# Optimization experiments

Hardware: AMD Instinct MI355X
Metric: run time of the kernel (lower is better)

The kernel has to match this reference:

```python
import jax, jax.numpy as jnp
import numpy as np

NUM_HEADS = 12


def setup_inputs() -> dict:
    key = jax.random.key(0)
    ks = jax.random.split(key, 6)
    C = 768
    hd = C // NUM_HEADS  # 64
    H = W = 32
    x = jax.random.normal(ks[0], (4, H, W, C), dtype=jnp.float32)
    # Linear weights stored as (in, out) so y = x @ W (+ b)
    Wqkv = jax.random.normal(ks[1], (C, 3 * C), dtype=jnp.float32) * 0.02
    Wproj = jax.random.normal(ks[2], (C, C), dtype=jnp.float32) * 0.02
    bproj = jax.random.normal(ks[3], (C,), dtype=jnp.float32) * 0.02
    rel_pos_h = jax.random.normal(ks[4], (2 * H - 1, hd), dtype=jnp.float32) * 0.02
    rel_pos_w = jax.random.normal(ks[5], (2 * W - 1, hd), dtype=jnp.float32) * 0.02
    return {"x": x, "Wqkv": Wqkv, "Wproj": Wproj, "bproj": bproj,
            "rel_pos_h": rel_pos_h, "rel_pos_w": rel_pos_w}


def _get_rel_pos(size: int, rel_pos: jnp.ndarray) -> jnp.ndarray:
    # q_size == k_size == size; table already has 2*size-1 entries -> no interpolation
    coords = jnp.arange(size)[:, None] - jnp.arange(size)[None, :] + (size - 1)
    return rel_pos[coords]  # (size, size, head_dim)


def reference(x, Wqkv, Wproj, bproj, rel_pos_h, rel_pos_w):
    B, H, W, C = x.shape
    hn = NUM_HEADS
    hd = C // hn
    scale = hd ** (-0.5)
    S = H * W

    qkv = x @ Wqkv                                   # (B,H,W,3C)
    qkv = qkv.reshape(B, S, 3, hn, hd)
    qkv = jnp.transpose(qkv, (2, 0, 3, 1, 4)).reshape(3, B * hn, S, hd)
    q, k, v = qkv[0], qkv[1], qkv[2]                 # each (B*hn, S, hd)

    # decomposed relative position bias
    Rh = _get_rel_pos(H, rel_pos_h)                  # (H,H,hd)
    Rw = _get_rel_pos(W, rel_pos_w)                  # (W,W,hd)
    r_q = q.reshape(B * hn, H, W, hd)
    rel_h = jnp.einsum('bhwc,hkc->bhwk', r_q, Rh)    # (B*hn,H,W,H)
    rel_w = jnp.einsum('bhwc,wkc->bhwk', r_q, Rw)    # (B*hn,H,W,W)
    bias = rel_h[..., :, None] + rel_w[..., None, :] # (B*hn,H,W,H,W)
    bias = bias.reshape(B * hn, S, S)

    scores = scale * jnp.einsum('bqc,bkc->bqk', q, k) + bias
    attn = jax.nn.softmax(scores, axis=-1)
    out = jnp.einsum('bqk,bkc->bqc', attn, v)        # (B*hn,S,hd)

    out = out.reshape(B, hn, H, W, hd)
    out = jnp.transpose(out, (0, 2, 3, 1, 4)).reshape(B, H, W, C)
    return out @ Wproj + bproj
```

## Files before the change

kernel.cpp:

```cpp
#include <hip/hip_runtime.h>
#include <stddef.h>

typedef __bf16 bf16x8 __attribute__((ext_vector_type(8)));
typedef __bf16 bf16x4 __attribute__((ext_vector_type(4)));
typedef _Float16 f16x4 __attribute__((ext_vector_type(4)));
typedef float  f32x4  __attribute__((ext_vector_type(4)));

#define MFMA16(a, b, c) __builtin_amdgcn_mfma_f32_16x16x32_bf16((a), (b), (c), 0, 0, 0)
#define MFMA16H(a, b, c) __builtin_amdgcn_mfma_f32_16x16x16f16((a), (b), (c), 0, 0, 0)

__device__ __forceinline__ void gload_lds16(const void* gsrc, void* ldst) {
    __builtin_amdgcn_global_load_lds(
        (__attribute__((address_space(1))) void*)gsrc,
        (__attribute__((address_space(3))) void*)ldst,
        16, 0, 0);
}

__global__ void prep_kernel(const float* __restrict__ x, __bf16* __restrict__ xbf,
                            const float* __restrict__ Wqkv, __bf16* __restrict__ WqkvT,
                            const float* __restrict__ Wproj, __bf16* __restrict__ WprojT) {
    __shared__ float tile[32][33];
    const int bx = blockIdx.x, tid = threadIdx.x;
    if (bx < 3072) {
        int i = bx * 256 + tid;
        float4 v = ((const float4*)x)[i];
        bf16x4 o = {(__bf16)v.x, (__bf16)v.y, (__bf16)v.z, (__bf16)v.w};
        ((bf16x4*)xbf)[i] = o;
        return;
    }
    const float* in; __bf16* out; int R, C, c0, r0;
    if (bx < 4800) { int bb = bx - 3072; in = Wqkv;  out = WqkvT;  R = 768; C = 2304;
                     c0 = (bb % 72) * 32; r0 = (bb / 72) * 32; }
    else           { int bb = bx - 4800; in = Wproj; out = WprojT; R = 768; C = 768;
                     c0 = (bb % 24) * 32; r0 = (bb / 24) * 32; }
    const int tx = tid & 31, ty = tid >> 5;
#pragma unroll
    for (int i = 0; i < 32; i += 8)
        tile[ty + i][tx] = in[(size_t)(r0 + ty + i) * C + c0 + tx];
    __syncthreads();
#pragma unroll
    for (int i = 0; i < 32; i += 8)
        out[(size_t)(c0 + ty + i) * R + r0 + tx] = (__bf16)tile[tx][ty + i];
}

__device__ __forceinline__ void gemm_core_bk64(
    const __bf16* __restrict__ A, const __bf16* __restrict__ Bt, int K,
    int m0, int n0, __bf16* aT, __bf16* bT, f32x4 acc[4][4]) {
    const int tid  = threadIdx.x;
    const int wid  = tid >> 6, lane = tid & 63;
    const int quad = lane >> 4, l16 = lane & 15;
    const int wm = (wid >> 1) * 64, wn = (wid & 1) * 64;
    const int r_in = lane >> 3;
    const int cswz = ((lane & 7) ^ r_in) * 8;
    const __bf16* gA = A  + (size_t)(m0 + wid * 8 + r_in) * K + cswz;
    const __bf16* gB = Bt + (size_t)(n0 + wid * 8 + r_in) * K + cswz;
    const int sA = (l16 & 7);
    for (int k0 = 0; k0 < K; k0 += 64) {
        __syncthreads();
#pragma unroll
        for (int j = 0; j < 4; j++) {
            gload_lds16(gA + (size_t)(j * 32) * K + k0, aT + (j * 32 + wid * 8) * 64);
            gload_lds16(gB + (size_t)(j * 32) * K + k0, bT + (j * 32 + wid * 8) * 64);
        }
        __syncthreads();
#pragma unroll
        for (int kh = 0; kh < 2; kh++) {
            bf16x8 af[4], bfr[4];
#pragma unroll
            for (int t = 0; t < 4; t++) {
                const int slot = ((kh * 4 + quad) ^ sA) << 3;
                af[t]  = *(const bf16x8*)(aT + (wm + t * 16 + l16) * 64 + slot);
                bfr[t] = *(const bf16x8*)(bT + (wn + t * 16 + l16) * 64 + slot);
            }
#pragma unroll
            for (int rt = 0; rt < 4; rt++)
#pragma unroll
                for (int ct = 0; ct < 4; ct++)
                    acc[rt][ct] = MFMA16(af[rt], bfr[ct], acc[rt][ct]);
        }
    }
}

__global__ __launch_bounds__(256, 3)
void gemm_qkv_kernel(const __bf16* __restrict__ A, const __bf16* __restrict__ Bt,
                     __bf16* __restrict__ qb, __bf16* __restrict__ kb,
                     _Float16* __restrict__ vtb) {
    __shared__ __bf16 aT[8192], bT[8192];
    f32x4 acc[4][4];
#pragma unroll
    for (int i = 0; i < 4; i++)
#pragma unroll
        for (int j = 0; j < 4; j++) { f32x4 z = {0.f, 0.f, 0.f, 0.f}; acc[i][j] = z; }
    const int m0 = blockIdx.x * 128, n0 = blockIdx.y * 128;
    gemm_core_bk64(A, Bt, 768, m0, n0, aT, bT, acc);
    const int tid = threadIdx.x, wid = tid >> 6, lane = tid & 63;
    const int quad = lane >> 4, l16 = lane & 15;
    const int wm = (wid >> 1) * 64, wn = (wid & 1) * 64;
#pragma unroll
    for (int rt = 0; rt < 4; rt++)
#pragma unroll
        for (int ct = 0; ct < 4; ct++) {
            const int ng = n0 + wn + ct * 16 + l16;
            const int which = ng / 768;
            const int rem = ng - which * 768;
            const int hh = rem >> 6, d = rem & 63;
#pragma unroll
            for (int r = 0; r < 4; r++) {
                const int mg = m0 + wm + rt * 16 + quad * 4 + r;
                const int b = mg >> 10, s = mg & 1023;
                const int bh = b * 12 + hh;
                if (which == 0)      qb[((size_t)bh * 1024 + s) * 64 + d] = (__bf16)acc[rt][ct][r];
                else if (which == 1) kb[((size_t)bh * 1024 + s) * 64 + d] = (__bf16)acc[rt][ct][r];
                else                 vtb[((size_t)bh * 64 + d) * 1024 + s] = (_Float16)acc[rt][ct][r];
            }
        }
}

__global__ __launch_bounds__(256, 3)
void gemm_proj_kernel(const __bf16* __restrict__ A, const __bf16* __restrict__ Bt,
                      const float* __restrict__ bias, float* __restrict__ out) {
    __shared__ __bf16 aT[8192], bT[8192];
    f32x4 acc[4][4];
#pragma unroll
    for (int i = 0; i < 4; i++)
#pragma unroll
        for (int j = 0; j < 4; j++) { f32x4 z = {0.f, 0.f, 0.f, 0.f}; acc[i][j] = z; }
    const int m0 = blockIdx.x * 128, n0 = blockIdx.y * 128;
    gemm_core_bk64(A, Bt, 768, m0, n0, aT, bT, acc);
    const int tid = threadIdx.x, wid = tid >> 6, lane = tid & 63;
    const int quad = lane >> 4, l16 = lane & 15;
    const int wm = (wid >> 1) * 64, wn = (wid & 1) * 64;
#pragma unroll
    for (int rt = 0; rt < 4; rt++)
#pragma unroll
        for (int ct = 0; ct < 4; ct++) {
            const int ng = n0 + wn + ct * 16 + l16;
            const float bb = bias[ng];
#pragma unroll
            for (int r = 0; r < 4; r++) {
                const int mg = m0 + wm + rt * 16 + quad * 4 + r;
                out[(size_t)mg * 768 + ng] = acc[rt][ct][r] + bb;
            }
        }
}

__global__ __launch_bounds__(256, 3)
void attn_kernel(const __bf16* __restrict__ q, const __bf16* __restrict__ kk,
                 const _Float16* __restrict__ vt, const float* __restrict__ rph,
                 const float* __restrict__ rpw, __bf16* __restrict__ aout) {
    __shared__ __bf16   kbuf2[2][4096];
    __shared__ _Float16 vbuf2[2][4096];
    __shared__ float    relh[64][33];
    const int tid = threadIdx.x, wid = tid >> 6, lane = tid & 63;
    const int quad = lane >> 4, l16 = lane & 15;
    const int bh = blockIdx.x, qt = blockIdx.y;
    const int b = bh / 12, hh = bh - b * 12;
    const int q0 = qt * 64;
    const int w0 = wid * 16;
    const int h = qt * 2 + (wid >> 1);

    const __bf16* qp = q + ((size_t)bh * 1024 + q0 + w0 + l16) * 64;
    bf16x8 aq0 = *(const bf16x8*)(qp + quad * 8);
    bf16x8 aq1 = *(const bf16x8*)(qp + 32 + quad * 8);

    float* Dw = ((float*)kbuf2) + wid * 1024;
#pragma unroll
    for (int ct = 0; ct < 4; ct++) {
        int j = ct * 16 + l16; if (j > 62) j = 62;
        const float* tb = rpw + (size_t)j * 64;
        float4 t0 = *(const float4*)(tb + quad * 8);
        float4 t1 = *(const float4*)(tb + quad * 8 + 4);
        float4 t2 = *(const float4*)(tb + 32 + quad * 8);
        float4 t3 = *(const float4*)(tb + 32 + quad * 8 + 4);
        bf16x8 b0 = {(__bf16)t0.x, (__bf16)t0.y, (__bf16)t0.z, (__bf16)t0.w,
                     (__bf16)t1.x, (__bf16)t1.y, (__bf16)t1.z, (__bf16)t1.w};
        bf16x8 b1 = {(__bf16)t2.x, (__bf16)t2.y, (__bf16)t2.z, (__bf16)t2.w,
                     (__bf16)t3.x, (__bf16)t3.y, (__bf16)t3.z, (__bf16)t3.w};
        f32x4 z = {0.f, 0.f, 0.f, 0.f};
        z = MFMA16(aq0, b0, z);
        z = MFMA16(aq1, b1, z);
#pragma unroll
        for (int i = 0; i < 4; i++)
            Dw[(quad * 4 + i) * 64 + ct * 16 + l16] = z[i];
    }
#pragma unroll
    for (int ct = 0; ct < 2; ct++) {
        const int tr = h - (ct * 16 + l16) + 31;
        const float* tb = rph + (size_t)tr * 64;
        float4 t0 = *(const float4*)(tb + quad * 8);
        float4 t1 = *(const float4*)(tb + quad * 8 + 4);
        float4 t2 = *(const float4*)(tb + 32 + quad * 8);
        float4 t3 = *(const float4*)(tb + 32 + quad * 8 + 4);
        bf16x8 b0 = {(__bf16)t0.x, (__bf16)t0.y, (__bf16)t0.z, (__bf16)t0.w,
                     (__bf16)t1.x, (__bf16)t1.y, (__bf16)t1.z, (__bf16)t1.w};
        bf16x8 b1 = {(__bf16)t2.x, (__bf16)t2.y, (__bf16)t2.z, (__bf16)t2.w,
                     (__bf16)t3.x, (__bf16)t3.y, (__bf16)t3.z, (__bf16)t3.w};
        f32x4 z = {0.f, 0.f, 0.f, 0.f};
        z = MFMA16(aq0, b0, z);
        z = MFMA16(aq1, b1, z);
#pragma unroll
        for (int i = 0; i < 4; i++)
            relh[w0 + quad * 4 + i][ct * 16 + l16] = z[i];
    }
    const int wq = (wid & 1) * 16 + l16;
    float bw[2][4];
#pragma unroll
    for (int hf = 0; hf < 2; hf++)
#pragma unroll
        for (int r = 0; r < 4; r++)
            bw[hf][r] = Dw[l16 * 64 + wq + 31 - hf * 16 - quad * 4 - r];
    __syncthreads();

    float l_run = 0.f;
    f32x4 o_acc[4];
#pragma unroll
    for (int t = 0; t < 4; t++) { f32x4 z = {0.f, 0.f, 0.f, 0.f}; o_acc[t] = z; }

    const __bf16*   kg0 = kk + (size_t)bh * 65536;
    const _Float16* vg0 = vt + (size_t)bh * 65536;
    const int cbase = wid * 2;
    const int srow = lane >> 3;
    const int scol = ((lane & 7) ^ srow) * 8;
    const int swz0 = ((quad ^ (l16 & 7)) << 3);
    const int swz1 = (((quad | 4) ^ (l16 & 7)) << 3);
    const int l7 = l16 & 7, qhi = quad >> 1, qlo = (quad & 1) * 4;

    auto stage = [&](int buf, int kt) {
        const __bf16*   kg = kg0 + kt * 4096;
        const _Float16* vg = vg0 + kt * 64;
        __bf16*   kb_ = &kbuf2[buf][0];
        _Float16* vb_ = &vbuf2[buf][0];
#pragma unroll
        for (int j = 0; j < 2; j++) {
            const int c = cbase + j;
            gload_lds16(kg + (c * 8 + srow) * 64 + scol, kb_ + c * 512);
            gload_lds16(vg + (size_t)(c * 8 + srow) * 1024 + scol, vb_ + c * 512);
        }
    };

    stage(0, 0);
    for (int kt = 0; kt < 16; kt++) {
        const int cur = kt & 1;
        __syncthreads();
        if (kt < 15) stage(1 - cur, kt + 1);
        const __bf16*   kbuf = &kbuf2[cur][0];
        const _Float16* vbuf = &vbuf2[cur][0];

        f32x4 sacc[4];
#pragma unroll
        for (int ct = 0; ct < 4; ct++) {
            const int key = ct * 16 + l16;
            bf16x8 bk0 = *(const bf16x8*)(kbuf + key * 64 + swz0);
            bf16x8 bk1 = *(const bf16x8*)(kbuf + key * 64 + swz1);
            f32x4 z = {0.f, 0.f, 0.f, 0.f};
            z = MFMA16(bk0, aq0, z);
            z = MFMA16(bk1, aq1, z);
            sacc[ct] = z;
        }

        const float bh0 = relh[w0 + l16][kt * 2];
        const float bh1 = relh[w0 + l16][kt * 2 + 1];
        f16x4 pf[4];
#pragma unroll
        for (int ct = 0; ct < 4; ct++) {
            const float bhc = (ct < 2) ? bh0 : bh1;
#pragma unroll
            for (int r = 0; r < 4; r++) {
                float sv = fmaf(sacc[ct][r], 0.125f, bhc + bw[ct & 1][r]);
                float p = __expf(sv);
                l_run += p;
                pf[ct][r] = (_Float16)p;
            }
        }

#pragma unroll
        for (int dt = 0; dt < 4; dt++) {
            const int vrow = (dt * 16 + l16) * 64;
#pragma unroll
            for (int ct = 0; ct < 4; ct++) {
                const int slot = (ct * 2 + qhi) ^ l7;
                f16x4 vf = *(const f16x4*)(vbuf + vrow + slot * 8 + qlo);
                o_acc[dt] = MFMA16H(vf, pf[ct], o_acc[dt]);
            }
        }
    }

    l_run += __shfl_xor(l_run, 16);
    l_run += __shfl_xor(l_run, 32);
    const float inv = 1.f / l_run;
    const int srow_o = q0 + w0 + l16;
#pragma unroll
    for (int dt = 0; dt < 4; dt++) {
        bf16x4 ov = {(__bf16)(o_acc[dt][0] * inv), (__bf16)(o_acc[dt][1] * inv),
                     (__bf16)(o_acc[dt][2] * inv), (__bf16)(o_acc[dt][3] * inv)};
        *(bf16x4*)&aout[((size_t)b * 1024 + srow_o) * 768 + hh * 64 + dt * 16 + quad * 4] = ov;
    }
}

extern "C" void kernel_launch(void* const* d_in, const int* in_sizes, int n_in,
                              void* d_out, int out_size, void* d_ws, size_t ws_size,
                              hipStream_t stream) {
    const float* x     = (const float*)d_in[0];
    const float* Wqkv  = (const float*)d_in[1];
    const float* Wproj = (const float*)d_in[2];
    const float* bproj = (const float*)d_in[3];
    const float* rph   = (const float*)d_in[4];
    const float* rpw   = (const float*)d_in[5];
    float* out = (float*)d_out;
    char* ws = (char*)d_ws;

    __bf16*   xbf    = (__bf16*)(ws);
    __bf16*   WqkvT  = (__bf16*)(ws + 6291456);
    __bf16*   WprojT = (__bf16*)(ws + 9830400);
    __bf16*   qb     = (__bf16*)(ws + 11010048);
    __bf16*   kb     = (__bf16*)(ws + 17301504);
    _Float16* vtb    = (_Float16*)(ws + 23592960);
    __bf16*   aob    = (__bf16*)(ws + 29884416);

    prep_kernel<<<dim3(5376), dim3(256), 0, stream>>>(x, xbf, Wqkv, WqkvT, Wproj, WprojT);
    gemm_qkv_kernel<<<dim3(32, 18), dim3(256), 0, stream>>>(xbf, WqkvT, qb, kb, vtb);
    attn_kernel<<<dim3(48, 16), dim3(256), 0, stream>>>(qb, kb, vtb, rph, rpw, aob);
    gemm_proj_kernel<<<dim3(32, 6), dim3(256), 0, stream>>>(aob, WprojT, bproj, out);
}
```

Before: 150.5 us.

## Give each attention wave two query row tiles to reuse K/V fragments

```diff
diff --git a/kernel.cpp b/kernel.cpp
--- a/kernel.cpp
+++ b/kernel.cpp
@@ -8,6 +8,7 @@
 
 #define MFMA16(a, b, c) __builtin_amdgcn_mfma_f32_16x16x32_bf16((a), (b), (c), 0, 0, 0)
 #define MFMA16H(a, b, c) __builtin_amdgcn_mfma_f32_16x16x16f16((a), (b), (c), 0, 0, 0)
+#define LOG2E 1.4426950408889634f
 
 __device__ __forceinline__ void gload_lds16(const void* gsrc, void* ldst) {
     __builtin_amdgcn_global_load_lds(
@@ -144,7 +145,7 @@
         }
 }
 
-__global__ __launch_bounds__(256, 3)
+__global__ __launch_bounds__(128, 2)
 void attn_kernel(const __bf16* __restrict__ q, const __bf16* __restrict__ kk,
                  const _Float16* __restrict__ vt, const float* __restrict__ rph,
                  const float* __restrict__ rpw, __bf16* __restrict__ aout) {
@@ -156,14 +157,18 @@
     const int bh = blockIdx.x, qt = blockIdx.y;
     const int b = bh / 12, hh = bh - b * 12;
     const int q0 = qt * 64;
-    const int w0 = wid * 16;
-    const int h = qt * 2 + (wid >> 1);
-
-    const __bf16* qp = q + ((size_t)bh * 1024 + q0 + w0 + l16) * 64;
-    bf16x8 aq0 = *(const bf16x8*)(qp + quad * 8);
-    bf16x8 aq1 = *(const bf16x8*)(qp + 32 + quad * 8);
-
-    float* Dw = ((float*)kbuf2) + wid * 1024;
+    const int w0 = wid * 32;
+    const int h = qt * 2 + wid;
+
+    bf16x8 aq[2][2];
+#pragma unroll
+    for (int rt = 0; rt < 2; rt++) {
+        const __bf16* qp = q + ((size_t)bh * 1024 + q0 + w0 + rt * 16 + l16) * 64;
+        aq[rt][0] = *(const bf16x8*)(qp + quad * 8);
+        aq[rt][1] = *(const bf16x8*)(qp + 32 + quad * 8);
+    }
+
+    float* Dw = ((float*)kbuf2) + wid * 2048;
 #pragma unroll
     for (int ct = 0; ct < 4; ct++) {
         int j = ct * 16 + l16; if (j > 62) j = 62;
@@ -176,12 +181,15 @@
                      (__bf16)t1.x, (__bf16)t1.y, (__bf16)t1.z, (__bf16)t1.w};
         bf16x8 b1 = {(__bf16)t2.x, (__bf16)t2.y, (__bf16)t2.z, (__bf16)t2.w,
                      (__bf16)t3.x, (__bf16)t3.y, (__bf16)t3.z, (__bf16)t3.w};
-        f32x4 z = {0.f, 0.f, 0.f, 0.f};
-        z = MFMA16(aq0, b0, z);
-        z = MFMA16(aq1, b1, z);
-#pragma unroll
-        for (int i = 0; i < 4; i++)
-            Dw[(quad * 4 + i) * 64 + ct * 16 + l16] = z[i];
+#pragma unroll
+        for (int rt = 0; rt < 2; rt++) {
+            f32x4 z = {0.f, 0.f, 0.f, 0.f};
+            z = MFMA16(aq[rt][0], b0, z);
+            z = MFMA16(aq[rt][1], b1, z);
+#pragma unroll
+            for (int i = 0; i < 4; i++)
+                Dw[(rt * 16 + quad * 4 + i) * 64 + ct * 16 + l16] = z[i];
+        }
     }
 #pragma unroll
     for (int ct = 0; ct < 2; ct++) {
@@ -195,35 +203,44 @@
                      (__bf16)t1.x, (__bf16)t1.y, (__bf16)t1.z, (__bf16)t1.w};
         bf16x8 b1 = {(__bf16)t2.x, (__bf16)t2.y, (__bf16)t2.z, (__bf16)t2.w,
                      (__bf16)t3.x, (__bf16)t3.y, (__bf16)t3.z, (__bf16)t3.w};
-        f32x4 z = {0.f, 0.f, 0.f, 0.f};
-        z = MFMA16(aq0, b0, z);
-        z = MFMA16(aq1, b1, z);
-#pragma unroll
-        for (int i = 0; i < 4; i++)
-            relh[w0 + quad * 4 + i][ct * 16 + l16] = z[i];
-    }
-    const int wq = (wid & 1) * 16 + l16;
-    float bw[2][4];
-#pragma unroll
-    for (int hf = 0; hf < 2; hf++)
-#pragma unroll
-        for (int r = 0; r < 4; r++)
-            bw[hf][r] = Dw[l16 * 64 + wq + 31 - hf * 16 - quad * 4 - r];
+#pragma unroll
+        for (int rt = 0; rt < 2; rt++) {
+            f32x4 z = {0.f, 0.f, 0.f, 0.f};
+            z = MFMA16(aq[rt][0], b0, z);
+            z = MFMA16(aq[rt][1], b1, z);
+#pragma unroll
+            for (int i = 0; i < 4; i++)
+                relh[w0 + rt * 16 + quad * 4 + i][ct * 16 + l16] = z[i] * LOG2E;
+        }
+    }
+    float bw[2][2][4];
+#pragma unroll
+    for (int rt = 0; rt < 2; rt++) {
+        const int rl = rt * 16 + l16;
+#pragma unroll
+        for (int hf = 0; hf < 2; hf++)
+#pragma unroll
+            for (int r = 0; r < 4; r++)
+                bw[rt][hf][r] = LOG2E * Dw[rl * 64 + rl + 31 - hf * 16 - quad * 4 - r];
+    }
     __syncthreads();
 
-    float l_run = 0.f;
-    f32x4 o_acc[4];
-#pragma unroll
-    for (int t = 0; t < 4; t++) { f32x4 z = {0.f, 0.f, 0.f, 0.f}; o_acc[t] = z; }
+    float l_run[2] = {0.f, 0.f};
+    f32x4 o_acc[2][4];
+#pragma unroll
+    for (int rt = 0; rt < 2; rt++)
+#pragma unroll
+        for (int t = 0; t < 4; t++) { f32x4 z = {0.f, 0.f, 0.f, 0.f}; o_acc[rt][t] = z; }
 
     const __bf16*   kg0 = kk + (size_t)bh * 65536;
     const _Float16* vg0 = vt + (size_t)bh * 65536;
-    const int cbase = wid * 2;
+    const int cbase = wid * 4;
     const int srow = lane >> 3;
     const int scol = ((lane & 7) ^ srow) * 8;
     const int swz0 = ((quad ^ (l16 & 7)) << 3);
     const int swz1 = (((quad | 4) ^ (l16 & 7)) << 3);
     const int l7 = l16 & 7, qhi = quad >> 1, qlo = (quad & 1) * 4;
+    const float SC = 0.125f * LOG2E;
 
     auto stage = [&](int buf, int kt) {
         const __bf16*   kg = kg0 + kt * 4096;
@@ -231,7 +248,7 @@
         __bf16*   kb_ = &kbuf2[buf][0];
         _Float16* vb_ = &vbuf2[buf][0];
 #pragma unroll
-        for (int j = 0; j < 2; j++) {
+        for (int j = 0; j < 4; j++) {
             const int c = cbase + j;
             gload_lds16(kg + (c * 8 + srow) * 64 + scol, kb_ + c * 512);
             gload_lds16(vg + (size_t)(c * 8 + srow) * 1024 + scol, vb_ + c * 512);
@@ -246,30 +263,40 @@
         const __bf16*   kbuf = &kbuf2[cur][0];
         const _Float16* vbuf = &vbuf2[cur][0];
 
-        f32x4 sacc[4];
+        bf16x8 bk[4][2];
 #pragma unroll
         for (int ct = 0; ct < 4; ct++) {
             const int key = ct * 16 + l16;
-            bf16x8 bk0 = *(const bf16x8*)(kbuf + key * 64 + swz0);
-            bf16x8 bk1 = *(const bf16x8*)(kbuf + key * 64 + swz1);
-            f32x4 z = {0.f, 0.f, 0.f, 0.f};
-            z = MFMA16(bk0, aq0, z);
-            z = MFMA16(bk1, aq1, z);
-            sacc[ct] = z;
-        }
-
-        const float bh0 = relh[w0 + l16][kt * 2];
-        const float bh1 = relh[w0 + l16][kt * 2 + 1];
-        f16x4 pf[4];
-#pragma unroll
-        for (int ct = 0; ct < 4; ct++) {
-            const float bhc = (ct < 2) ? bh0 : bh1;
-#pragma unroll
-            for (int r = 0; r < 4; r++) {
-                float sv = fmaf(sacc[ct][r], 0.125f, bhc + bw[ct & 1][r]);
-                float p = __expf(sv);
-                l_run += p;
-                pf[ct][r] = (_Float16)p;
+            bk[ct][0] = *(const bf16x8*)(kbuf + key * 64 + swz0);
+            bk[ct][1] = *(const bf16x8*)(kbuf + key * 64 + swz1);
+        }
+
+        f32x4 sacc[2][4];
+#pragma unroll
+        for (int rt = 0; rt < 2; rt++)
+#pragma unroll
+            for (int ct = 0; ct < 4; ct++) {
+                f32x4 z = {0.f, 0.f, 0.f, 0.f};
+                z = MFMA16(bk[ct][0], aq[rt][0], z);
+                z = MFMA16(bk[ct][1], aq[rt][1], z);
+                sacc[rt][ct] = z;
+            }
+
+        f16x4 pf[2][4];
+#pragma unroll
+        for (int rt = 0; rt < 2; rt++) {
+            const float bh0 = relh[w0 + rt * 16 + l16][kt * 2];
+            const float bh1 = relh[w0 + rt * 16 + l16][kt * 2 + 1];
+#pragma unroll
+            for (int ct = 0; ct < 4; ct++) {
+                const float bhc = (ct < 2) ? bh0 : bh1;
+#pragma unroll
+                for (int r = 0; r < 4; r++) {
+                    float sv = fmaf(sacc[rt][ct][r], SC, bhc + bw[rt][ct & 1][r]);
+                    float p = exp2f(sv);
+                    l_run[rt] += p;
+                    pf[rt][ct][r] = (_Float16)p;
+                }
             }
         }
 
@@ -280,20 +307,25 @@
             for (int ct = 0; ct < 4; ct++) {
                 const int slot = (ct * 2 + qhi) ^ l7;
                 f16x4 vf = *(const f16x4*)(vbuf + vrow + slot * 8 + qlo);
-                o_acc[dt] = MFMA16H(vf, pf[ct], o_acc[dt]);
-            }
-        }
-    }
-
-    l_run += __shfl_xor(l_run, 16);
-    l_run += __shfl_xor(l_run, 32);
-    const float inv = 1.f / l_run;
-    const int srow_o = q0 + w0 + l16;
-#pragma unroll
-    for (int dt = 0; dt < 4; dt++) {
-        bf16x4 ov = {(__bf16)(o_acc[dt][0] * inv), (__bf16)(o_acc[dt][1] * inv),
-                     (__bf16)(o_acc[dt][2] * inv), (__bf16)(o_acc[dt][3] * inv)};
-        *(bf16x4*)&aout[((size_t)b * 1024 + srow_o) * 768 + hh * 64 + dt * 16 + quad * 4] = ov;
+                o_acc[0][dt] = MFMA16H(vf, pf[0][ct], o_acc[0][dt]);
+                o_acc[1][dt] = MFMA16H(vf, pf[1][ct], o_acc[1][dt]);
+            }
+        }
+    }
+
+#pragma unroll
+    for (int rt = 0; rt < 2; rt++) {
+        float s = l_run[rt];
+        s += __shfl_xor(s, 16);
+        s += __shfl_xor(s, 32);
+        const float inv = 1.f / s;
+        const int srow_o = q0 + w0 + rt * 16 + l16;
+#pragma unroll
+        for (int dt = 0; dt < 4; dt++) {
+            bf16x4 ov = {(__bf16)(o_acc[rt][dt][0] * inv), (__bf16)(o_acc[rt][dt][1] * inv),
+                         (__bf16)(o_acc[rt][dt][2] * inv), (__bf16)(o_acc[rt][dt][3] * inv)};
+            *(bf16x4*)&aout[((size_t)b * 1024 + srow_o) * 768 + hh * 64 + dt * 16 + quad * 4] = ov;
+        }
     }
 }
 
@@ -319,6 +351,6 @@
 
     prep_kernel<<<dim3(5376), dim3(256), 0, stream>>>(x, xbf, Wqkv, WqkvT, Wproj, WprojT);
     gemm_qkv_kernel<<<dim3(32, 18), dim3(256), 0, stream>>>(xbf, WqkvT, qb, kb, vtb);
-    attn_kernel<<<dim3(48, 16), dim3(256), 0, stream>>>(qb, kb, vtb, rph, rpw, aob);
+    attn_kernel<<<dim3(48, 16), dim3(128), 0, stream>>>(qb, kb, vtb, rph, rpw, aob);
     gemm_proj_kernel<<<dim3(32, 6), dim3(256), 0, stream>>>(aob, WprojT, bproj, out);
 }
```

Result: slower. 157.3 us (+4.5%).
